# Optimization experiments

Measured on AMD Instinct MI355X. Metric: run time of the kernel, lower is better.

The kernel has to match this reference:

```python
import jax, jax.numpy as jnp
import numpy as np

B, T_Q, T_C = 4, 2048, 2048
Q_DIM = C_DIM = H_DIM = OUT_DIM = 1024
N_HEADS = 16
D = H_DIM // N_HEADS


def setup_inputs() -> dict:
    key = jax.random.key(0)
    ks = jax.random.split(key, 10)
    s_q = 1.0 / np.sqrt(Q_DIM)
    s_c = 1.0 / np.sqrt(C_DIM)
    s_h = 1.0 / np.sqrt(H_DIM)
    return {
        "query": jax.random.normal(ks[0], (B, T_Q, Q_DIM), jnp.float32),
        "context": jax.random.normal(ks[1], (B, T_C, C_DIM), jnp.float32),
        "Wq": jax.random.uniform(ks[2], (Q_DIM, H_DIM), jnp.float32, -s_q, s_q),
        "bq": jax.random.uniform(ks[3], (H_DIM,), jnp.float32, -s_q, s_q),
        "Wk": jax.random.uniform(ks[4], (C_DIM, H_DIM), jnp.float32, -s_c, s_c),
        "bk": jax.random.uniform(ks[5], (H_DIM,), jnp.float32, -s_c, s_c),
        "Wv": jax.random.uniform(ks[6], (C_DIM, H_DIM), jnp.float32, -s_c, s_c),
        "bv": jax.random.uniform(ks[7], (H_DIM,), jnp.float32, -s_c, s_c),
        "Wo": jax.random.uniform(ks[8], (H_DIM, OUT_DIM), jnp.float32, -s_h, s_h),
        "bo": jax.random.uniform(ks[9], (OUT_DIM,), jnp.float32, -s_h, s_h),
    }


def reference(query, context, Wq, bq, Wk, bk, Wv, bv, Wo, bo):
    Bq, Tq, _ = query.shape
    _, Tc, _ = context.shape
    # project and split heads: [B, H, T, D]
    q = (query @ Wq + bq).reshape(Bq, Tq, N_HEADS, D).transpose(0, 2, 1, 3)
    k = (context @ Wk + bk).reshape(Bq, Tc, N_HEADS, D).transpose(0, 2, 1, 3)
    v = (context @ Wv + bv).reshape(Bq, Tc, N_HEADS, D).transpose(0, 2, 1, 3)
    scores = jnp.einsum("bhqd,bhkd->bhqk", q, k) / jnp.sqrt(jnp.float32(D))
    probs = jax.nn.softmax(scores, axis=-1)
    attn = jnp.einsum("bhqk,bhkd->bhqd", probs, v)  # dropout p=0 -> identity
    attn = attn.transpose(0, 2, 1, 3).reshape(Bq, Tq, N_HEADS * D)
    return attn @ Wo + bo
```

## Files before the change

kernel.cpp:

```cpp
#include <hip/hip_runtime.h>
#include <hip/hip_bf16.h>
#include <cstdint>

typedef __attribute__((ext_vector_type(8))) short short8;
typedef __attribute__((ext_vector_type(4))) short short4_t;
typedef __attribute__((ext_vector_type(4))) float f32x4;

#define MFMA16(a, b, c) __builtin_amdgcn_mfma_f32_16x16x32_bf16(a, b, c, 0, 0, 0)
#define MFMA16K16(a, b, c) __builtin_amdgcn_mfma_f32_16x16x16bf16_1k(a, b, c, 0, 0, 0)

__device__ __forceinline__ short f2b(float f) {
    union { float fp; unsigned u; } un; un.fp = f;
    unsigned r = un.u + 0x7fffu + ((un.u >> 16) & 1u);
    return (short)(r >> 16);
}

#if __has_builtin(__builtin_amdgcn_cvt_pk_bf16_f32)
__device__ __forceinline__ unsigned pk_bf16(float a, float b) {
    auto r = __builtin_amdgcn_cvt_pk_bf16_f32(a, b);
    unsigned u; __builtin_memcpy(&u, &r, 4); return u;
}
#else
__device__ __forceinline__ unsigned pk_bf16(float a, float b) {
    return (unsigned)(unsigned short)f2b(a) | ((unsigned)(unsigned short)f2b(b) << 16);
}
#endif

union pk4_u { unsigned u2[2]; short4_t s; };

typedef const __attribute__((address_space(1))) unsigned g_as1;
typedef __attribute__((address_space(3))) unsigned l_as3;
__device__ __forceinline__ void gll16(const ushort* g, ushort* l) {
    __builtin_amdgcn_global_load_lds((g_as1*)g, (l_as3*)l, 16, 0, 0);
}

__global__ __launch_bounds__(256) void in_cvt_kernel(
    const float* __restrict__ q, const float* __restrict__ c,
    ushort* __restrict__ qb, ushort* __restrict__ cb)
{
    const float* src = blockIdx.y ? c : q;
    ushort* dst = blockIdx.y ? cb : qb;
    size_t i = ((size_t)blockIdx.x * 256 + threadIdx.x) * 8;
    float4 v0 = *(const float4*)&src[i];
    float4 v1 = *(const float4*)&src[i + 4];
    uint4 o;
    o.x = pk_bf16(v0.x, v0.y); o.y = pk_bf16(v0.z, v0.w);
    o.z = pk_bf16(v1.x, v1.y); o.w = pk_bf16(v1.z, v1.w);
    *(uint4*)&dst[i] = o;
}

__global__ __launch_bounds__(256) void wt_cvt_kernel(
    const float* __restrict__ Wq, const float* __restrict__ Wk,
    const float* __restrict__ Wv, const float* __restrict__ Wo,
    ushort* __restrict__ wt)
{
    __shared__ float Ts[64 * 65];
    const int z = blockIdx.z;
    const float* W = (z == 0) ? Wq : (z == 1) ? Wk : (z == 2) ? Wv : Wo;
    ushort* WT = wt + (size_t)z * (1024 * 1024);
    const int n0 = blockIdx.x * 64, k0 = blockIdx.y * 64;
    const int tid = threadIdx.x;

#pragma unroll
    for (int rr = 0; rr < 4; ++rr) {
        int u = tid + rr * 256;
        int r = u >> 4, c = (u & 15) * 4;
        float4 v = *(const float4*)&W[(size_t)(k0 + r) * 1024 + n0 + c];
        Ts[r * 65 + c + 0] = v.x; Ts[r * 65 + c + 1] = v.y;
        Ts[r * 65 + c + 2] = v.z; Ts[r * 65 + c + 3] = v.w;
    }
    __syncthreads();
#pragma unroll
    for (int rr = 0; rr < 4; ++rr) {
        int u = tid + rr * 256;
        int rn = u >> 4, ck = (u & 15) * 4;
        short4_t o;
        o[0] = f2b(Ts[(ck + 0) * 65 + rn]);
        o[1] = f2b(Ts[(ck + 1) * 65 + rn]);
        o[2] = f2b(Ts[(ck + 2) * 65 + rn]);
        o[3] = f2b(Ts[(ck + 3) * 65 + rn]);
        *(short4_t*)&WT[(size_t)(n0 + rn) * 1024 + k0 + ck] = o;
    }
}

template <int MODE>
__global__ __launch_bounds__(256) void gemm_kernel(
    const ushort* __restrict__ Ag, const ushort* __restrict__ BT,
    const float* __restrict__ bias, void* __restrict__ Outp, float scale)
{
    __shared__ ushort As[128 * 64];
    __shared__ ushort Bs[128 * 64];
    const int tid = threadIdx.x;
    const int w = tid >> 6, lane = tid & 63;
    const int ln = tid & 15, quad = (tid >> 4) & 3;
    const int wm = w >> 1, wn = w & 1;
    const int m0 = blockIdx.y * 128, n0 = blockIdx.x * 128;

    int offA[4], offB[4], lseg[4];
#pragma unroll
    for (int rr = 0; rr < 4; ++rr) {
        int idx = (rr * 4 + w) * 64 + lane;
        int r = idx >> 3, cst = idx & 7, csrc = cst ^ (r & 7);
        offA[rr] = (m0 + r) * 1024 + csrc * 8;
        offB[rr] = (n0 + r) * 1024 + csrc * 8;
        lseg[rr] = (rr * 4 + w) * 512;
    }

    f32x4 acc[4][4] = {};

    for (int kk = 0; kk < 1024; kk += 64) {
        __syncthreads();
#pragma unroll
        for (int rr = 0; rr < 4; ++rr)
            gll16(&Ag[(size_t)(offA[rr] + kk)], &As[lseg[rr]]);
#pragma unroll
        for (int rr = 0; rr < 4; ++rr)
            gll16(&BT[(size_t)(offB[rr] + kk)], &Bs[lseg[rr]]);
        __syncthreads();

#pragma unroll
        for (int ks = 0; ks < 2; ++ks) {
            short8 af[4], bfr[4];
#pragma unroll
            for (int i = 0; i < 4; ++i)
                af[i] = *(const short8*)&As[(wm * 64 + i * 16 + ln) * 64 +
                                            ((ks * 4 + quad) ^ (ln & 7)) * 8];
#pragma unroll
            for (int j = 0; j < 4; ++j)
                bfr[j] = *(const short8*)&Bs[(wn * 64 + j * 16 + ln) * 64 +
                                             ((ks * 4 + quad) ^ (ln & 7)) * 8];
#pragma unroll
            for (int i = 0; i < 4; ++i)
#pragma unroll
                for (int j = 0; j < 4; ++j)
                    acc[i][j] = MFMA16(af[i], bfr[j], acc[i][j]);
        }
    }

#pragma unroll
    for (int j = 0; j < 4; ++j) {
        int n = n0 + wn * 64 + j * 16 + ln;
        float bv = bias[n];
#pragma unroll
        for (int i = 0; i < 4; ++i) {
            int mb = m0 + wm * 64 + i * 16 + quad * 4;
            if (MODE == 3) {
                float* Out = (float*)Outp;
#pragma unroll
                for (int r = 0; r < 4; ++r)
                    Out[(size_t)(mb + r) * 1024 + n] = acc[i][j][r] + bv;
            } else {
                ushort* Out = (ushort*)Outp;
                int h = n >> 6, d = n & 63;
#pragma unroll
                for (int r = 0; r < 4; ++r) {
                    int m = mb + r, b = m >> 11, t = m & 2047;
                    Out[(((size_t)(b * 16 + h) * 2048 + t) << 6) + d] =
                        (ushort)f2b((acc[i][j][r] + bv) * scale);
                }
            }
        }
    }
}

__global__ __launch_bounds__(256) void kv_kernel(
    const ushort* __restrict__ Cb, const ushort* __restrict__ WTk,
    const ushort* __restrict__ WTv,
    const float* __restrict__ bk, const float* __restrict__ bv,
    ushort* __restrict__ Kw, ushort* __restrict__ Vtw)
{
    __shared__ ushort As[128 * 64];
    __shared__ ushort Bs[128 * 64];
    const int tid = threadIdx.x;
    const int w = tid >> 6, lane = tid & 63;
    const int ln = tid & 15, quad = (tid >> 4) & 3;
    const int wm = w >> 1, wn = w & 1;
    const int z = blockIdx.x >> 3;
    const int n0 = (blockIdx.x & 7) * 128;
    const int m0 = blockIdx.y * 128;
    const ushort* BT = z ? WTv : WTk;

    int offA[4], offB[4], lseg[4];
#pragma unroll
    for (int rr = 0; rr < 4; ++rr) {
        int idx = (rr * 4 + w) * 64 + lane;
        int r = idx >> 3, cst = idx & 7, csrc = cst ^ (r & 7);
        offA[rr] = (m0 + r) * 1024 + csrc * 8;
        offB[rr] = (n0 + r) * 1024 + csrc * 8;
        lseg[rr] = (rr * 4 + w) * 512;
    }

    f32x4 acc[4][4] = {};

    for (int kk = 0; kk < 1024; kk += 64) {
        __syncthreads();
#pragma unroll
        for (int rr = 0; rr < 4; ++rr)
            gll16(&Cb[(size_t)(offA[rr] + kk)], &As[lseg[rr]]);
#pragma unroll
        for (int rr = 0; rr < 4; ++rr)
            gll16(&BT[(size_t)(offB[rr] + kk)], &Bs[lseg[rr]]);
        __syncthreads();

#pragma unroll
        for (int ks = 0; ks < 2; ++ks) {
            short8 af[4], bfr[4];
#pragma unroll
            for (int i = 0; i < 4; ++i)
                af[i] = *(const short8*)&As[(wm * 64 + i * 16 + ln) * 64 +
                                            ((ks * 4 + quad) ^ (ln & 7)) * 8];
#pragma unroll
            for (int j = 0; j < 4; ++j)
                bfr[j] = *(const short8*)&Bs[(wn * 64 + j * 16 + ln) * 64 +
                                             ((ks * 4 + quad) ^ (ln & 7)) * 8];
#pragma unroll
            for (int i = 0; i < 4; ++i)
#pragma unroll
                for (int j = 0; j < 4; ++j)
                    acc[i][j] = MFMA16(af[i], bfr[j], acc[i][j]);
        }
    }

#pragma unroll
    for (int j = 0; j < 4; ++j) {
        int n = n0 + wn * 64 + j * 16 + ln;
        int h = n >> 6, d = n & 63;
        if (z == 0) {
            float bvv = bk[n];
#pragma unroll
            for (int i = 0; i < 4; ++i) {
                int mb = m0 + wm * 64 + i * 16 + quad * 4;
#pragma unroll
                for (int r = 0; r < 4; ++r) {
                    int m = mb + r, b = m >> 11, t = m & 2047;
                    Kw[(((size_t)(b * 16 + h) * 2048 + t) << 6) + d] =
                        (ushort)f2b(acc[i][j][r] + bvv);
                }
            }
        } else {
            float bvv = bv[n];
#pragma unroll
            for (int i = 0; i < 4; ++i) {
                int mb = m0 + wm * 64 + i * 16 + quad * 4;
                int b = mb >> 11, t = mb & 2047;
                short4_t o;
                o[0] = f2b(acc[i][j][0] + bvv); o[1] = f2b(acc[i][j][1] + bvv);
                o[2] = f2b(acc[i][j][2] + bvv); o[3] = f2b(acc[i][j][3] + bvv);
                *(short4_t*)&Vtw[(((size_t)((b * 16 + h) * 64 + d)) << 11) + t] = o;
            }
        }
    }
}

__global__ __launch_bounds__(256, 4) void attn_kernel(
    const ushort* __restrict__ Qw, const ushort* __restrict__ Kw,
    const ushort* __restrict__ Vtw, ushort* __restrict__ attn)
{
    __shared__ ushort Ks[4096];
    __shared__ ushort Vts[4096];

    const int tid = threadIdx.x;
    const int w = tid >> 6, lane = tid & 63;
    const int ln = tid & 15, quad = (tid >> 4) & 3;
    const int bh = blockIdx.y, b = bh >> 4, h = bh & 15;
    const int qt = blockIdx.x;

    const ushort* Qg = Qw + (size_t)bh * 131072 + (size_t)qt * 8192;
    const ushort* Kg = Kw + (size_t)bh * 131072;
    const ushort* Vg = Vtw + (size_t)bh * 131072;

    short8 bq[2][2];
#pragma unroll
    for (int qs = 0; qs < 2; ++qs)
#pragma unroll
        for (int ks = 0; ks < 2; ++ks)
            bq[qs][ks] = *(const short8*)&Qg[(w * 32 + qs * 16 + ln) * 64 + ks * 32 + quad * 8];

    int offK[2], offV[2], lseg[2];
#pragma unroll
    for (int rr = 0; rr < 2; ++rr) {
        int idx = (rr * 4 + w) * 64 + lane;
        int r = idx >> 3, cst = idx & 7, csrc = cst ^ (r & 7);
        offK[rr] = r * 64 + csrc * 8;
        offV[rr] = r * 2048 + csrc * 8;
        lseg[rr] = (rr * 4 + w) * 512;
    }

    const short4_t ones = {(short)0x3F80, (short)0x3F80, (short)0x3F80, (short)0x3F80};

    f32x4 Of[2][4] = {};
    f32x4 lac[2] = {};

    for (int kt = 0; kt < 32; ++kt) {
        __syncthreads();
#pragma unroll
        for (int rr = 0; rr < 2; ++rr)
            gll16(&Kg[kt * 4096 + offK[rr]], &Ks[lseg[rr]]);
#pragma unroll
        for (int rr = 0; rr < 2; ++rr)
            gll16(&Vg[kt * 64 + offV[rr]], &Vts[lseg[rr]]);
        __syncthreads();

        f32x4 sa[4][2];
#pragma unroll
        for (int kv = 0; kv < 4; ++kv) {
            short8 a0 = *(const short8*)&Ks[(kv * 16 + ln) * 64 + (quad ^ (ln & 7)) * 8];
            short8 a1 = *(const short8*)&Ks[(kv * 16 + ln) * 64 + ((4 + quad) ^ (ln & 7)) * 8];
#pragma unroll
            for (int qs = 0; qs < 2; ++qs) {
                f32x4 s = {};
                s = MFMA16(a0, bq[qs][0], s);
                s = MFMA16(a1, bq[qs][1], s);
                sa[kv][qs] = s;
            }
        }

        short4_t pf[4][2];
#pragma unroll
        for (int qs = 0; qs < 2; ++qs)
#pragma unroll
            for (int kv = 0; kv < 4; ++kv) {
                float p0 = __builtin_amdgcn_exp2f(sa[kv][qs][0]);
                float p1 = __builtin_amdgcn_exp2f(sa[kv][qs][1]);
                float p2 = __builtin_amdgcn_exp2f(sa[kv][qs][2]);
                float p3 = __builtin_amdgcn_exp2f(sa[kv][qs][3]);
                pk4_u pu;
                pu.u2[0] = pk_bf16(p0, p1);
                pu.u2[1] = pk_bf16(p2, p3);
                pf[kv][qs] = pu.s;
                lac[qs] = MFMA16K16(ones, pu.s, lac[qs]);
            }

#pragma unroll
        for (int kv = 0; kv < 4; ++kv) {
#pragma unroll
            for (int ds = 0; ds < 4; ++ds) {
                short4_t vf = *(const short4_t*)&Vts[(ds * 16 + ln) * 64 +
                    (((2 * kv + (quad >> 1)) ^ (ln & 7)) * 8) + (quad & 1) * 4];
#pragma unroll
                for (int qs = 0; qs < 2; ++qs)
                    Of[qs][ds] = MFMA16K16(vf, pf[kv][qs], Of[qs][ds]);
            }
        }
    }

#pragma unroll
    for (int qs = 0; qs < 2; ++qs) {
        float inv = __builtin_amdgcn_rcpf(lac[qs][0]);
        int t = qt * 128 + w * 32 + qs * 16 + ln;
        size_t base = ((size_t)(b * 2048 + t) << 10) + h * 64;
#pragma unroll
        for (int ds = 0; ds < 4; ++ds) {
            uint2 o;
            o.x = pk_bf16(Of[qs][ds][0] * inv, Of[qs][ds][1] * inv);
            o.y = pk_bf16(Of[qs][ds][2] * inv, Of[qs][ds][3] * inv);
            *(uint2*)&attn[base + ds * 16 + quad * 4] = o;
        }
    }
}

extern "C" void kernel_launch(void* const* d_in, const int* in_sizes, int n_in,
                              void* d_out, int out_size, void* d_ws, size_t ws_size,
                              hipStream_t stream)
{
    const float* query   = (const float*)d_in[0];
    const float* context = (const float*)d_in[1];
    const float* Wq = (const float*)d_in[2];
    const float* bq = (const float*)d_in[3];
    const float* Wk = (const float*)d_in[4];
    const float* bk = (const float*)d_in[5];
    const float* Wv = (const float*)d_in[6];
    const float* bv = (const float*)d_in[7];
    const float* Wo = (const float*)d_in[8];
    const float* bo = (const float*)d_in[9];

    char* ws = (char*)d_ws;
    ushort* WT  = (ushort*)ws;
    ushort* Qb  = (ushort*)(ws + 8388608);
    ushort* Qw  = (ushort*)(ws + 25165824);
    ushort* Kw  = (ushort*)(ws + 41943040);
    ushort* Vtw = (ushort*)(ws + 58720256);
    ushort* Aw  = Qb;
    ushort* Cb  = (ushort*)d_out;

    const float SCALE = 0.18033688011112042f;

    in_cvt_kernel<<<dim3(4096, 2), 256, 0, stream>>>(query, context, Qb, Cb);
    wt_cvt_kernel<<<dim3(16, 16, 4), 256, 0, stream>>>(Wq, Wk, Wv, Wo, WT);
    gemm_kernel<0><<<dim3(8, 64), 256, 0, stream>>>(Qb, WT + 0 * 1048576, bq, Qw, SCALE);
    kv_kernel<<<dim3(16, 64), 256, 0, stream>>>(Cb, WT + 1 * 1048576,
                                                WT + 2 * 1048576, bk, bv, Kw, Vtw);
    attn_kernel<<<dim3(16, 64), 256, 0, stream>>>(Qw, Kw, Vtw, Aw);
    gemm_kernel<3><<<dim3(8, 64), 256, 0, stream>>>(Aw, WT + 3 * 1048576, bo,
                                                    (float*)d_out, 1.0f);
}
```

Measured before the change: 324.3 us.

## Double-buffer K/V tiles in attention and remap block IDs for XCD locality

The attention kernel now keeps two LDS buffers for K and V. It prefetches the next tile with global-to-LDS loads while the current tile is computed, so each iteration needs one barrier instead of two. The grid is flattened to 1D and block IDs are remapped so that consecutive blocks spread over (b,h) in groups of 8. This aims to improve L2 reuse of K and V on MI355X's chiplet layout. LDS use doubles to 32KB per block, which may cut occupancy.

```diff
diff --git a/kernel.cpp b/kernel.cpp
--- a/kernel.cpp
+++ b/kernel.cpp
@@ -256,14 +256,16 @@
     const ushort* __restrict__ Qw, const ushort* __restrict__ Kw,
     const ushort* __restrict__ Vtw, ushort* __restrict__ attn)
 {
-    __shared__ ushort Ks[4096];
-    __shared__ ushort Vts[4096];
+    __shared__ ushort Ks[2][4096];
+    __shared__ ushort Vts[2][4096];
 
     const int tid = threadIdx.x;
     const int w = tid >> 6, lane = tid & 63;
     const int ln = tid & 15, quad = (tid >> 4) & 3;
-    const int bh = blockIdx.y, b = bh >> 4, h = bh & 15;
-    const int qt = blockIdx.x;
+    const int id = blockIdx.x;
+    const int qt = (id >> 3) & 15;
+    const int bh = (id & 7) | ((id >> 7) << 3);
+    const int b = bh >> 4, h = bh & 15;
 
     const ushort* Qg = Qw + (size_t)bh * 131072 + (size_t)qt * 8192;
     const ushort* Kg = Kw + (size_t)bh * 131072;
@@ -291,21 +293,28 @@
     f32x4 Of[2][4] = {};
     f32x4 lac[2] = {};
 
-    for (int kt = 0; kt < 32; ++kt) {
-        __syncthreads();
-#pragma unroll
-        for (int rr = 0; rr < 2; ++rr)
-            gll16(&Kg[kt * 4096 + offK[rr]], &Ks[lseg[rr]]);
-#pragma unroll
-        for (int rr = 0; rr < 2; ++rr)
-            gll16(&Vg[kt * 64 + offV[rr]], &Vts[lseg[rr]]);
-        __syncthreads();
+#pragma unroll
+    for (int rr = 0; rr < 2; ++rr) gll16(&Kg[offK[rr]], &Ks[0][lseg[rr]]);
+#pragma unroll
+    for (int rr = 0; rr < 2; ++rr) gll16(&Vg[offV[rr]], &Vts[0][lseg[rr]]);
+    __syncthreads();
+
+    auto body = [&](int kt, const ushort* Kc, const ushort* Vc,
+                    ushort* Kn, ushort* Vn) {
+        if (kt < 31) {
+#pragma unroll
+            for (int rr = 0; rr < 2; ++rr)
+                gll16(&Kg[(kt + 1) * 4096 + offK[rr]], &Kn[lseg[rr]]);
+#pragma unroll
+            for (int rr = 0; rr < 2; ++rr)
+                gll16(&Vg[(kt + 1) * 64 + offV[rr]], &Vn[lseg[rr]]);
+        }
 
         f32x4 sa[4][2];
 #pragma unroll
         for (int kv = 0; kv < 4; ++kv) {
-            short8 a0 = *(const short8*)&Ks[(kv * 16 + ln) * 64 + (quad ^ (ln & 7)) * 8];
-            short8 a1 = *(const short8*)&Ks[(kv * 16 + ln) * 64 + ((4 + quad) ^ (ln & 7)) * 8];
+            short8 a0 = *(const short8*)&Kc[(kv * 16 + ln) * 64 + (quad ^ (ln & 7)) * 8];
+            short8 a1 = *(const short8*)&Kc[(kv * 16 + ln) * 64 + ((4 + quad) ^ (ln & 7)) * 8];
 #pragma unroll
             for (int qs = 0; qs < 2; ++qs) {
                 f32x4 s = {};
@@ -335,13 +344,20 @@
         for (int kv = 0; kv < 4; ++kv) {
 #pragma unroll
             for (int ds = 0; ds < 4; ++ds) {
-                short4_t vf = *(const short4_t*)&Vts[(ds * 16 + ln) * 64 +
+                short4_t vf = *(const short4_t*)&Vc[(ds * 16 + ln) * 64 +
                     (((2 * kv + (quad >> 1)) ^ (ln & 7)) * 8) + (quad & 1) * 4];
 #pragma unroll
                 for (int qs = 0; qs < 2; ++qs)
                     Of[qs][ds] = MFMA16K16(vf, pf[kv][qs], Of[qs][ds]);
             }
         }
+
+        __syncthreads();
+    };
+
+    for (int kt = 0; kt < 32; kt += 2) {
+        body(kt,     Ks[0], Vts[0], Ks[1], Vts[1]);
+        body(kt + 1, Ks[1], Vts[1], Ks[0], Vts[0]);
     }
 
 #pragma unroll
@@ -390,7 +406,7 @@
     gemm_kernel<0><<<dim3(8, 64), 256, 0, stream>>>(Qb, WT + 0 * 1048576, bq, Qw, SCALE);
     kv_kernel<<<dim3(16, 64), 256, 0, stream>>>(Cb, WT + 1 * 1048576,
                                                 WT + 2 * 1048576, bk, bv, Kw, Vtw);
-    attn_kernel<<<dim3(16, 64), 256, 0, stream>>>(Qw, Kw, Vtw, Aw);
+    attn_kernel<<<dim3(1024), 256, 0, stream>>>(Qw, Kw, Vtw, Aw);
     gemm_kernel<3><<<dim3(8, 64), 256, 0, stream>>>(Aw, WT + 3 * 1048576, bo,
                                                     (float*)d_out, 1.0f);
 }
```

Measured after the change: 331.3 us. 2.2% more time.
